# Kernel optimization log

Measured on AMD Instinct MI355X. Metric: run time of the kernel, lower is better.

Reference implementation:

```python
import jax, jax.numpy as jnp
import numpy as np

EPS = 1e-8  # matches torch F.cosine_similarity eps


def setup_inputs() -> dict:
    key = jax.random.key(0)
    S, U, D = 2048, 10, 256  # speakers, utterances/speaker, embedding dim
    embeddings = jax.random.normal(key, (S * U, D), dtype=jnp.float32)
    labels = jnp.repeat(jnp.arange(S, dtype=jnp.int64), U)  # speaker-blocked, as the view() assumes
    return {"embeddings": embeddings, "labels": labels}


def reference(embeddings, labels):
    labels_np = np.asarray(labels)
    S = int(np.unique(labels_np).size)          # num_speakers (static)
    B, D = embeddings.shape
    U = B // S                                   # num_utterances
    E = embeddings.reshape(S, U, D)
    C = E.mean(axis=1)                           # (S, D) centroids
    En = E / jnp.maximum(jnp.linalg.norm(E, axis=-1, keepdims=True), EPS)
    Cn = C / jnp.maximum(jnp.linalg.norm(C, axis=-1, keepdims=True), EPS)
    sim = jnp.einsum('sud,kd->suk', En, Cn)      # (S, U, S) cosine similarities
    idx = jnp.arange(S)
    pos = sim[idx, :, idx]                       # (S, U) similarity to own centroid
    neg_mask = jnp.eye(S, dtype=bool)[:, None, :]  # mask out k == i
    neg = jnp.where(neg_mask, -jnp.inf, sim)
    lse = jax.nn.logsumexp(neg, axis=-1)         # (S, U)
    loss = jnp.mean(-pos + lse)
    return loss
```

## Files before the change

kernel.cpp:

```cpp
#include <hip/hip_runtime.h>
#include <math.h>

#define SS   2048
#define UU   10
#define DD   256
#define BB   (SS * UU)
#define EPSF 1e-8f

typedef __attribute__((ext_vector_type(8))) short   bf16x8;
typedef __attribute__((ext_vector_type(4))) float   floatx4;

__device__ static inline unsigned short f2bf(float f) {
    union { float f; unsigned u; } v; v.f = f;
    unsigned r = (v.u + 0x7FFFu + ((v.u >> 16) & 1u)) >> 16;
    return (unsigned short)r;
}

__device__ static inline void gl_lds16(const unsigned short* g, unsigned short* l) {
    __builtin_amdgcn_global_load_lds((const __attribute__((address_space(1))) void*)g,
                                     (__attribute__((address_space(3))) void*)l, 16, 0, 0);
}

__global__ __launch_bounds__(256) void prep_kernel(const float* __restrict__ E,
                                                   unsigned short* __restrict__ Enb,
                                                   unsigned short* __restrict__ Cnb,
                                                   float* __restrict__ sumexp,
                                                   float* __restrict__ out) {
    const int s   = blockIdx.x;
    const int wid = threadIdx.x >> 6, lane = threadIdx.x & 63;
    __shared__ float cent[4][256];
    __shared__ float sred[256];

    if (threadIdx.x < UU) sumexp[s * UU + threadIdx.x] = 0.f;
    if (s == 0 && threadIdx.x == 0) out[0] = 0.f;

    float cp0 = 0.f, cp1 = 0.f, cp2 = 0.f, cp3 = 0.f;
    for (int u = wid; u < UU; u += 4) {
        const size_t roff = (size_t)(s * UU + u) * DD;
        float4 v = ((const float4*)(E + roff))[lane];
        float ssq = v.x * v.x + v.y * v.y + v.z * v.z + v.w * v.w;
#pragma unroll
        for (int off = 32; off; off >>= 1) ssq += __shfl_xor(ssq, off, 64);
        const float rinv = 1.0f / fmaxf(sqrtf(ssq), EPSF);
        ushort4 o;
        o.x = f2bf(v.x * rinv); o.y = f2bf(v.y * rinv);
        o.z = f2bf(v.z * rinv); o.w = f2bf(v.w * rinv);
        ((ushort4*)(Enb + roff))[lane] = o;
        cp0 += v.x; cp1 += v.y; cp2 += v.z; cp3 += v.w;
    }
    cent[wid][lane * 4 + 0] = cp0;
    cent[wid][lane * 4 + 1] = cp1;
    cent[wid][lane * 4 + 2] = cp2;
    cent[wid][lane * 4 + 3] = cp3;
    __syncthreads();

    const int d = threadIdx.x;
    const float c = (cent[0][d] + cent[1][d] + cent[2][d] + cent[3][d]) * 0.1f;
    sred[d] = c * c;
    __syncthreads();
#pragma unroll
    for (int off = 128; off; off >>= 1) {
        if (d < off) sred[d] += sred[d + off];
        __syncthreads();
    }
    const float rinv = 1.0f / fmaxf(sqrtf(sred[0]), EPSF);
    Cnb[(size_t)s * DD + d] = f2bf(c * rinv);
}

#define BM 128
#define BN 128
#define BK 32
#define NCK 8
#define CHUNK (BM * BK)

__device__ __forceinline__ void chunk_mfma(const unsigned short* Ab,
                                           const unsigned short* Bb,
                                           const int* aoff, const int* boff,
                                           floatx4 (&acc)[4][4]) {
    bf16x8 af[4], bfr[4];
#pragma unroll
    for (int t = 0; t < 4; ++t) af[t]  = *(const bf16x8*)(Ab + aoff[t]);
#pragma unroll
    for (int t = 0; t < 4; ++t) bfr[t] = *(const bf16x8*)(Bb + boff[t]);
#pragma unroll
    for (int mt = 0; mt < 4; ++mt)
#pragma unroll
        for (int nt = 0; nt < 4; ++nt)
            acc[mt][nt] = __builtin_amdgcn_mfma_f32_16x16x32_bf16(af[mt], bfr[nt], acc[mt][nt], 0, 0, 0);
}

__global__ __launch_bounds__(256) void gemm_lse_kernel(const unsigned short* __restrict__ Enb,
                                                       const unsigned short* __restrict__ Cnb,
                                                       float* __restrict__ posArr,
                                                       float* __restrict__ sumexp) {
    __shared__ unsigned short As[2 * CHUNK];
    __shared__ unsigned short Bs[2 * CHUNK];

    const int tid  = threadIdx.x;
    const int wid  = tid >> 6, lane = tid & 63;
    const int l15  = lane & 15, quad = lane >> 4;
    const int wave_m = wid >> 1, wave_n = wid & 1;

    const int swz = (blockIdx.x & 7) * 320 + (blockIdx.x >> 3);
    const int bn = swz & 15;
    const int bm = swz >> 4;
    const int row0 = bm * BM, n0 = bn * BN;

    const int rl = lane >> 2;
    const int gf = ((lane & 3) ^ ((rl >> 1) & 3)) * 8;
    const unsigned short* gp[4];
    unsigned short* lp[4];
#pragma unroll
    for (int i = 0; i < 4; ++i) {
        const int c = wid * 4 + i;
        if (c < 8) {
            gp[i] = Enb + (size_t)(row0 + c * 16 + rl) * DD + gf;
            lp[i] = As + c * 512;
        } else {
            gp[i] = Cnb + (size_t)(n0 + (c - 8) * 16 + rl) * DD + gf;
            lp[i] = Bs + (c - 8) * 512;
        }
    }

    const int fswz = (quad ^ ((l15 >> 1) & 3)) * 8;
    int aoff[4], boff[4];
#pragma unroll
    for (int t = 0; t < 4; ++t) {
        aoff[t] = (wave_m * 64 + t * 16 + l15) * BK + fswz;
        boff[t] = (wave_n * 64 + t * 16 + l15) * BK + fswz;
    }

    floatx4 acc[4][4];
#pragma unroll
    for (int i = 0; i < 4; ++i)
#pragma unroll
        for (int j = 0; j < 4; ++j) acc[i][j] = (floatx4){0.f, 0.f, 0.f, 0.f};

#pragma unroll
    for (int i = 0; i < 4; ++i) gl_lds16(gp[i], lp[i]);
    __syncthreads();

#pragma unroll
    for (int t = 0; t < NCK; ++t) {
        const int buf = t & 1;
        if (t + 1 < NCK) {
#pragma unroll
            for (int i = 0; i < 4; ++i)
                gl_lds16(gp[i] + (t + 1) * BK, lp[i] + ((t + 1) & 1) * CHUNK);
        }
        chunk_mfma(As + buf * CHUNK, Bs + buf * CHUNK, aoff, boff, acc);
        __syncthreads();
    }

#pragma unroll
    for (int mt = 0; mt < 4; ++mt) {
        float rs[4] = {0.f, 0.f, 0.f, 0.f};
        const int growb = row0 + wave_m * 64 + mt * 16 + quad * 4;
#pragma unroll
        for (int nt = 0; nt < 4; ++nt) {
            const int col = n0 + wave_n * 64 + nt * 16 + l15;
#pragma unroll
            for (int r = 0; r < 4; ++r) {
                const int grow = growb + r;
                const float sim = acc[mt][nt][r];
                if (col == grow / UU) {
                    posArr[grow] = sim;
                } else {
                    rs[r] += __expf(sim);
                }
            }
        }
#pragma unroll
        for (int m = 1; m < 16; m <<= 1) {
#pragma unroll
            for (int r = 0; r < 4; ++r) rs[r] += __shfl_xor(rs[r], m, 64);
        }
        if (l15 == 0) {
#pragma unroll
            for (int r = 0; r < 4; ++r) atomicAdd(&sumexp[growb + r], rs[r]);
        }
    }
}

__global__ __launch_bounds__(256) void finalize_kernel(const float* __restrict__ posArr,
                                                       const float* __restrict__ sumexp,
                                                       float* __restrict__ out) {
    __shared__ float sred[256];
    const int tid = threadIdx.x;
    const int r = blockIdx.x * 256 + tid;
    sred[tid] = logf(sumexp[r]) - posArr[r];
    __syncthreads();
#pragma unroll
    for (int off = 128; off; off >>= 1) {
        if (tid < off) sred[tid] += sred[tid + off];
        __syncthreads();
    }
    if (tid == 0) atomicAdd(out, sred[0] * (1.0f / (float)BB));
}

extern "C" void kernel_launch(void* const* d_in, const int* in_sizes, int n_in,
                              void* d_out, int out_size, void* d_ws, size_t ws_size,
                              hipStream_t stream) {
    const float* E = (const float*)d_in[0];
    float* out = (float*)d_out;

    unsigned short* Enb = (unsigned short*)d_ws;
    unsigned short* Cnb = Enb + (size_t)BB * DD;
    float* posArr = (float*)(Cnb + (size_t)SS * DD);
    float* sumexp = posArr + BB;

    prep_kernel<<<SS, 256, 0, stream>>>(E, Enb, Cnb, sumexp, out);
    gemm_lse_kernel<<<(BB / BM) * (SS / BN), 256, 0, stream>>>(Enb, Cnb, posArr, sumexp);
    finalize_kernel<<<BB / 256, 256, 0, stream>>>(posArr, sumexp, out);
}
```

Measured before the change: 120.4 us.

## Deepen GEMM LDS pipeline to four buffers with explicit waitcnt and MFMA priority

The GEMM main loop moves from a double-buffered prefetch-one scheme to a four-slot ring that prefetches two chunks ahead. It uses explicit s_waitcnt vmcnt plus a raw barrier and a single sync per step, and raises wave priority around the MFMA block. The epilogue precomputes row labels and batches the shuffle reductions. The prep kernel replaces its LDS tree reduction with wave shuffles. The aim is to hide global-to-LDS load latency and cut barrier count, at the cost of doubling LDS use per block, which may reduce occupancy.

```diff
diff --git a/kernel.cpp b/kernel.cpp
--- a/kernel.cpp
+++ b/kernel.cpp
@@ -29,7 +29,7 @@
     const int s   = blockIdx.x;
     const int wid = threadIdx.x >> 6, lane = threadIdx.x & 63;
     __shared__ float cent[4][256];
-    __shared__ float sred[256];
+    __shared__ float part[4];
 
     if (threadIdx.x < UU) sumexp[s * UU + threadIdx.x] = 0.f;
     if (s == 0 && threadIdx.x == 0) out[0] = 0.f;
@@ -56,20 +56,19 @@
 
     const int d = threadIdx.x;
     const float c = (cent[0][d] + cent[1][d] + cent[2][d] + cent[3][d]) * 0.1f;
-    sred[d] = c * c;
+    float p = c * c;
+#pragma unroll
+    for (int off = 32; off; off >>= 1) p += __shfl_xor(p, off, 64);
+    if (lane == 0) part[wid] = p;
     __syncthreads();
-#pragma unroll
-    for (int off = 128; off; off >>= 1) {
-        if (d < off) sred[d] += sred[d + off];
-        __syncthreads();
-    }
-    const float rinv = 1.0f / fmaxf(sqrtf(sred[0]), EPSF);
+    const float tot = part[0] + part[1] + part[2] + part[3];
+    const float rinv = 1.0f / fmaxf(sqrtf(tot), EPSF);
     Cnb[(size_t)s * DD + d] = f2bf(c * rinv);
 }
 
-#define BM 128
-#define BN 128
-#define BK 32
+#define BM  128
+#define BN  128
+#define BK  32
 #define NCK 8
 #define CHUNK (BM * BK)
 
@@ -82,19 +81,21 @@
     for (int t = 0; t < 4; ++t) af[t]  = *(const bf16x8*)(Ab + aoff[t]);
 #pragma unroll
     for (int t = 0; t < 4; ++t) bfr[t] = *(const bf16x8*)(Bb + boff[t]);
+    __builtin_amdgcn_s_setprio(1);
 #pragma unroll
     for (int mt = 0; mt < 4; ++mt)
 #pragma unroll
         for (int nt = 0; nt < 4; ++nt)
             acc[mt][nt] = __builtin_amdgcn_mfma_f32_16x16x32_bf16(af[mt], bfr[nt], acc[mt][nt], 0, 0, 0);
+    __builtin_amdgcn_s_setprio(0);
 }
 
 __global__ __launch_bounds__(256) void gemm_lse_kernel(const unsigned short* __restrict__ Enb,
                                                        const unsigned short* __restrict__ Cnb,
                                                        float* __restrict__ posArr,
                                                        float* __restrict__ sumexp) {
-    __shared__ unsigned short As[2 * CHUNK];
-    __shared__ unsigned short Bs[2 * CHUNK];
+    __shared__ unsigned short As[4 * CHUNK];
+    __shared__ unsigned short Bs[4 * CHUNK];
 
     const int tid  = threadIdx.x;
     const int wid  = tid >> 6, lane = tid & 63;
@@ -138,46 +139,63 @@
 
 #pragma unroll
     for (int i = 0; i < 4; ++i) gl_lds16(gp[i], lp[i]);
-    __syncthreads();
-
-#pragma unroll
-    for (int t = 0; t < NCK; ++t) {
-        const int buf = t & 1;
-        if (t + 1 < NCK) {
-#pragma unroll
-            for (int i = 0; i < 4; ++i)
-                gl_lds16(gp[i] + (t + 1) * BK, lp[i] + ((t + 1) & 1) * CHUNK);
-        }
-        chunk_mfma(As + buf * CHUNK, Bs + buf * CHUNK, aoff, boff, acc);
-        __syncthreads();
-    }
-
+#pragma unroll
+    for (int i = 0; i < 4; ++i) gl_lds16(gp[i] + BK, lp[i] + CHUNK);
+
+#define GSTEP(T, VM, ISSUE)                                                  \
+    asm volatile("s_waitcnt vmcnt(" #VM ")" ::: "memory");                   \
+    __builtin_amdgcn_s_barrier();                                            \
+    __builtin_amdgcn_sched_barrier(0);                                       \
+    if (ISSUE) {                                                             \
+        _Pragma("unroll")                                                    \
+        for (int i = 0; i < 4; ++i)                                          \
+            gl_lds16(gp[i] + ((T) + 2) * BK, lp[i] + (((T) + 2) & 3) * CHUNK); \
+    }                                                                        \
+    chunk_mfma(As + ((T) & 3) * CHUNK, Bs + ((T) & 3) * CHUNK, aoff, boff, acc);
+
+    GSTEP(0, 4, 1) GSTEP(1, 4, 1) GSTEP(2, 4, 1) GSTEP(3, 4, 1)
+    GSTEP(4, 4, 1) GSTEP(5, 4, 1) GSTEP(6, 4, 0) GSTEP(7, 0, 0)
+#undef GSTEP
+
+    int lbl[4][4];
+    float rs[4][4];
 #pragma unroll
     for (int mt = 0; mt < 4; ++mt) {
-        float rs[4] = {0.f, 0.f, 0.f, 0.f};
+        const int growb = row0 + wave_m * 64 + mt * 16 + quad * 4;
+#pragma unroll
+        for (int r = 0; r < 4; ++r) {
+            lbl[mt][r] = (growb + r) / UU;
+            rs[mt][r]  = 0.f;
+        }
+    }
+#pragma unroll
+    for (int mt = 0; mt < 4; ++mt) {
         const int growb = row0 + wave_m * 64 + mt * 16 + quad * 4;
 #pragma unroll
         for (int nt = 0; nt < 4; ++nt) {
             const int col = n0 + wave_n * 64 + nt * 16 + l15;
 #pragma unroll
             for (int r = 0; r < 4; ++r) {
-                const int grow = growb + r;
                 const float sim = acc[mt][nt][r];
-                if (col == grow / UU) {
-                    posArr[grow] = sim;
+                if (col == lbl[mt][r]) {
+                    posArr[growb + r] = sim;
                 } else {
-                    rs[r] += __expf(sim);
+                    rs[mt][r] += __expf(sim);
                 }
             }
         }
+    }
+#pragma unroll
+    for (int mt = 0; mt < 4; ++mt) {
+        const int growb = row0 + wave_m * 64 + mt * 16 + quad * 4;
 #pragma unroll
         for (int m = 1; m < 16; m <<= 1) {
 #pragma unroll
-            for (int r = 0; r < 4; ++r) rs[r] += __shfl_xor(rs[r], m, 64);
+            for (int r = 0; r < 4; ++r) rs[mt][r] += __shfl_xor(rs[mt][r], m, 64);
         }
         if (l15 == 0) {
 #pragma unroll
-            for (int r = 0; r < 4; ++r) atomicAdd(&sumexp[growb + r], rs[r]);
+            for (int r = 0; r < 4; ++r) atomicAdd(&sumexp[growb + r], rs[mt][r]);
         }
     }
 }
```

After: 123.5 us. 1.03x slower.
